# Kernel optimization log

Hardware: AMD Instinct MI355X
Metric: run time of the kernel (lower is better)

Reference implementation:

```python
import jax, jax.numpy as jnp
import numpy as np

B, S, D = 2, 2048, 2560
H, HD = 32, 80           # n_head, head_dim = n_embd // n_head
RD = 32                  # rotary_dim (partial rotary, phi-style)
ROPE_BASE = 10000.0


def _rope_cache(seqlen, rotary_dim):
    # inv_freq = 1 / base^(2i/d); freqs = outer(t, inv_freq)  -> [S, RD//2]
    inv_freq = 1.0 / (ROPE_BASE ** (jnp.arange(0, rotary_dim, 2, dtype=jnp.float32) / rotary_dim))
    t = jnp.arange(seqlen, dtype=jnp.float32)
    freqs = jnp.outer(t, inv_freq)
    return jnp.cos(freqs), jnp.sin(freqs)


def setup_inputs() -> dict:
    key = jax.random.key(0)
    k0, k1, k2, k3, k4 = jax.random.split(key, 5)
    x = jax.random.normal(k0, (B, S, D), dtype=jnp.float32)
    wqkv_w = jax.random.normal(k1, (3 * D, D), dtype=jnp.float32) * 0.02
    wqkv_b = jax.random.normal(k2, (3 * D,), dtype=jnp.float32) * 0.02
    out_w = jax.random.normal(k3, (D, D), dtype=jnp.float32) * 0.02
    out_b = jax.random.normal(k4, (D,), dtype=jnp.float32) * 0.02
    return {"x": x, "wqkv_w": wqkv_w, "wqkv_b": wqkv_b, "out_w": out_w, "out_b": out_b}


def _attention_core(x, wqkv_w, wqkv_b, out_w, out_b):
    b, s, d = x.shape
    qkv = (x @ wqkv_w.T + wqkv_b).reshape(b, s, 3, H, HD)  # [B,S,3,H,HD]

    cos, sin = _rope_cache(s, RD)            # [S, RD//2]
    c = cos[:, None, :]                       # [S,1,RD//2]
    si = sin[:, None, :]

    def rot(t):  # partial NeoX-style rotary on first RD dims; t: [B,S,H,HD]
        t_rot, t_pass = t[..., :RD], t[..., RD:]
        t1, t2 = t_rot[..., : RD // 2], t_rot[..., RD // 2 :]
        return jnp.concatenate([t1 * c - t2 * si, t1 * si + t2 * c, t_pass], axis=-1)

    q = rot(qkv[:, :, 0])                     # [B,S,H,HD]
    k = rot(qkv[:, :, 1])
    v = qkv[:, :, 2]

    # fp32 scores = q @ (k * scale)^T, causal mask filled with -10000.0 (as in source)
    scale = 1.0 / np.sqrt(HD).astype(np.float32)
    scores = jnp.einsum("bqhd,bkhd->bhqk", q, k * scale)  # [B,H,S,S]
    causal_mask = jnp.arange(s)[None, :] > jnp.arange(s)[:, None]  # cols > rows
    scores = jnp.where(causal_mask, jnp.float32(-10000.0), scores)
    attn = jax.nn.softmax(scores, axis=-1)
    ctx = jnp.einsum("bhqk,bkhd->bqhd", attn, v).reshape(b, s, d)
    return ctx @ out_w.T + out_b


def reference(x, wqkv_w, wqkv_b, out_w, out_b):
    return _attention_core(x, wqkv_w, wqkv_b, out_w, out_b)
```

## Files before the change

### kernel.cpp

```cpp
#include <hip/hip_runtime.h>
#include <cstdint>
#include <cstddef>

#define B_  2
#define S_  2048
#define D_  2560
#define H_  32
#define HD_ 80

typedef __attribute__((ext_vector_type(8))) short  short8;
typedef __attribute__((ext_vector_type(4))) float  floatx4;

__device__ __forceinline__ float b2f(unsigned short u) {
  union { unsigned int i; float f; } x; x.i = ((unsigned int)u) << 16; return x.f;
}
__device__ __forceinline__ unsigned short f2bf(float f) {
  union { float f; unsigned int i; } x; x.f = f;
  unsigned int u = x.i;
  return (unsigned short)((u + 0x7fffu + ((u >> 16) & 1u)) >> 16);
}

__global__ void cvt_kernel(const float* __restrict__ in, unsigned short* __restrict__ out, int n4) {
  int i = blockIdx.x * 256 + threadIdx.x;
  if (i >= n4) return;
  const float4 v = ((const float4*)in)[i];
  ushort4 r;
  r.x = f2bf(v.x); r.y = f2bf(v.y); r.z = f2bf(v.z); r.w = f2bf(v.w);
  ((ushort4*)out)[i] = r;
}

#define GLOAD_LDS16(g, l)                                                      \
  __builtin_amdgcn_global_load_lds(                                            \
      (const __attribute__((address_space(1))) void*)(g),                      \
      (__attribute__((address_space(3))) void*)(l), 16, 0, 0)

template <int OUT_BF16>
__global__ __launch_bounds__(256)
void gemm_bt(const unsigned short* __restrict__ A,
             const unsigned short* __restrict__ B,
             const float* __restrict__ bias,
             void* __restrict__ Cv,
             const int M, const int N, const int K) {
  __shared__ unsigned short As[128 * 32];
  __shared__ unsigned short Bs[128 * 32];
  const int tid  = threadIdx.x;
  const int wave = tid >> 6;
  const int lane = tid & 63;
  const int wm   = (wave & 1) << 6;
  const int wn   = (wave >> 1) << 6;
  const int row0 = (int)blockIdx.y << 7;
  const int col0 = (int)blockIdx.x << 7;
  const unsigned short* Ab = A + (size_t)row0 * K;
  const unsigned short* Bb = B + (size_t)col0 * K;
  const int srow = wave * 16 + (lane >> 2);
  const int scol = (lane & 3) << 3;
  const int fr = lane & 15;
  const int fq = (lane >> 4) << 3;
  floatx4 acc[4][4] = {};

  for (int k0 = 0; k0 < K; k0 += 32) {
    __syncthreads();
    GLOAD_LDS16(Ab + (size_t)srow        * K + (k0 + scol), &As[wave * 512]);
    GLOAD_LDS16(Ab + (size_t)(srow + 64) * K + (k0 + scol), &As[2048 + wave * 512]);
    GLOAD_LDS16(Bb + (size_t)srow        * K + (k0 + scol), &Bs[wave * 512]);
    GLOAD_LDS16(Bb + (size_t)(srow + 64) * K + (k0 + scol), &Bs[2048 + wave * 512]);
    __syncthreads();
    short8 aF[4], bF[4];
#pragma unroll
    for (int i = 0; i < 4; i++) aF[i] = *(const short8*)(&As[(wm + i * 16 + fr) * 32 + fq]);
#pragma unroll
    for (int i = 0; i < 4; i++) bF[i] = *(const short8*)(&Bs[(wn + i * 16 + fr) * 32 + fq]);
#pragma unroll
    for (int mi = 0; mi < 4; mi++)
#pragma unroll
      for (int ni = 0; ni < 4; ni++)
        acc[mi][ni] = __builtin_amdgcn_mfma_f32_16x16x32_bf16(aF[mi], bF[ni], acc[mi][ni], 0, 0, 0);
  }

  const int cr = (lane >> 4) << 2;
  const int cn = lane & 15;
  unsigned short* Cb = (unsigned short*)Cv;
  float* Cf = (float*)Cv;
#pragma unroll
  for (int ni = 0; ni < 4; ni++) {
    const int col = col0 + wn + ni * 16 + cn;
    const float bv = bias[col];
#pragma unroll
    for (int mi = 0; mi < 4; mi++) {
      const int rowb = row0 + wm + mi * 16 + cr;
#pragma unroll
      for (int r = 0; r < 4; r++) {
        const float v = acc[mi][ni][r] + bv;
        const size_t idx = (size_t)(rowb + r) * N + col;
        if (OUT_BF16) Cb[idx] = f2bf(v);
        else          Cf[idx] = v;
      }
    }
  }
}

__global__ void rope_kernel(const unsigned short* __restrict__ qkv,
                            unsigned short* __restrict__ Q,
                            unsigned short* __restrict__ K) {
  const int idx = blockIdx.x * 256 + threadIdx.x;
  if (idx >= B_ * S_ * H_) return;
  const int h = idx & (H_ - 1);
  const int s = (idx >> 5) & (S_ - 1);
  const int b = idx >> 16;
  const unsigned short* row = qkv + (size_t)(b * S_ + s) * (3 * D_);
  const size_t obase = ((size_t)(b * H_ + h) * S_ + s) * HD_;

  float cc[16], ssn[16];
#pragma unroll
  for (int i = 0; i < 16; i++) {
    const float ang = (float)s * exp2f((float)i * -0.83048202372184059f);
    ssn[i] = sinf(ang);
    cc[i]  = cosf(ang);
  }
  {
    const float QS = 0.11180339887498949f * 1.4426950408889634f;
    const uint4* src = (const uint4*)(row + h * HD_);
    float f[80], g[80];
#pragma unroll
    for (int i = 0; i < 10; i++) {
      uint4 t = src[i];
      const unsigned short* w = (const unsigned short*)&t;
#pragma unroll
      for (int j = 0; j < 8; j++) f[i * 8 + j] = b2f(w[j]);
    }
#pragma unroll
    for (int i = 0; i < 16; i++) {
      g[i]      = f[i] * cc[i] - f[i + 16] * ssn[i];
      g[i + 16] = f[i] * ssn[i] + f[i + 16] * cc[i];
    }
#pragma unroll
    for (int i = 32; i < 80; i++) g[i] = f[i];
    uint4* dst = (uint4*)(Q + obase);
#pragma unroll
    for (int i = 0; i < 10; i++) {
      uint4 t;
      unsigned short* w = (unsigned short*)&t;
#pragma unroll
      for (int j = 0; j < 8; j++) w[j] = f2bf(g[i * 8 + j] * QS);
      dst[i] = t;
    }
  }
  {
    const uint4* src = (const uint4*)(row + (H_ + h) * HD_);
    float f[32], g[32];
#pragma unroll
    for (int i = 0; i < 4; i++) {
      uint4 t = src[i];
      const unsigned short* w = (const unsigned short*)&t;
#pragma unroll
      for (int j = 0; j < 8; j++) f[i * 8 + j] = b2f(w[j]);
    }
#pragma unroll
    for (int i = 0; i < 16; i++) {
      g[i]      = f[i] * cc[i] - f[i + 16] * ssn[i];
      g[i + 16] = f[i] * ssn[i] + f[i + 16] * cc[i];
    }
    uint4* dst = (uint4*)(K + obase);
#pragma unroll
    for (int i = 0; i < 4; i++) {
      uint4 t;
      unsigned short* w = (unsigned short*)&t;
#pragma unroll
      for (int j = 0; j < 8; j++) w[j] = f2bf(g[i * 8 + j]);
      dst[i] = t;
    }
#pragma unroll
    for (int i = 4; i < 10; i++) dst[i] = src[i];
  }
}

__global__ __launch_bounds__(256)
void vtrans_kernel(const unsigned short* __restrict__ qkv, unsigned short* __restrict__ Vt) {
  __shared__ unsigned short T[64][88];
  const int tid = threadIdx.x;
  const int bh = blockIdx.y;
  const int b = bh >> 5, h = bh & 31;
  const int tile = blockIdx.x;
  const int s0 = tile * 64;
  for (int t = tid; t < 640; t += 256) {
    const int r = t / 10, c = t % 10;
    const size_t src = ((size_t)((b * S_ + s0 + r) * 3) + 2) * D_ + h * HD_ + c * 8;
    *(uint4*)&T[r][c * 8] = *(const uint4*)&qkv[src];
  }
  __syncthreads();
  unsigned short* tb = Vt + ((size_t)bh * 32 + tile) * (80 * 72);
  for (int t = tid; t < 640; t += 256) {
    const int d = t / 8, sc = t % 8;
    uint4 o;
    unsigned short* w = (unsigned short*)&o;
#pragma unroll
    for (int j = 0; j < 8; j++) w[j] = T[sc * 8 + j][d];
    *(uint4*)&tb[d * 72 + sc * 8] = o;
  }
}

__global__ __launch_bounds__(256, 4)
void attn_mfma(const unsigned short* __restrict__ Qg,
               const unsigned short* __restrict__ Kg,
               const unsigned short* __restrict__ Vtg,
               unsigned short* __restrict__ ctx) {
  __shared__ unsigned short Ks[64 * 80];
  __shared__ unsigned short Vs[80 * 72];
  __shared__ unsigned short Ps[4][32 * 72];

  const int tid  = threadIdx.x;
  const int wave = tid >> 6;
  const int lane = tid & 63;
  const int fr   = lane & 15;
  const int fg   = lane >> 4;
  const int bh   = blockIdx.y;
  const int qt   = (int)gridDim.x - 1 - (int)blockIdx.x;
  const int qbase = (qt << 7) + wave * 32;

  const unsigned short* Qrow  = Qg  + (size_t)bh * S_ * HD_;
  const unsigned short* Krow  = Kg  + (size_t)bh * S_ * HD_;
  const unsigned short* Vtile = Vtg + (size_t)bh * 32 * (80 * 72);

  short8 qf[2][3];
  const short8 zfrag = {};
#pragma unroll
  for (int mi = 0; mi < 2; mi++) {
    const unsigned short* qp = Qrow + (size_t)(qbase + mi * 16 + fr) * HD_;
    qf[mi][0] = *(const short8*)&qp[fg * 8];
    qf[mi][1] = *(const short8*)&qp[32 + fg * 8];
    qf[mi][2] = (fg < 2) ? *(const short8*)&qp[64 + fg * 8] : zfrag;
  }

  floatx4 accO[2][5] = {};
  float l_part[2][4] = {};

  const int nch = 2 * qt + 2;
  for (int c = 0; c < nch; c++) {
    const int k0 = c * 64;
    __syncthreads();
    {
      const unsigned short* Kt = Krow + (size_t)k0 * HD_;
      for (int i = wave; i < 10; i += 4)
        GLOAD_LDS16(Kt + i * 512 + lane * 8, &Ks[i * 512]);
    }
    {
      const unsigned short* Vt = Vtile + (size_t)c * (80 * 72);
      for (int i = wave; i < 12; i += 4) {
        const int off = (i < 11) ? i * 512 : 5248;
        GLOAD_LDS16(Vt + off + lane * 8, &Vs[off]);
      }
    }
    __syncthreads();

    floatx4 accS[2][4] = {};
#pragma unroll
    for (int ni = 0; ni < 4; ni++) {
      const unsigned short* kp = &Ks[(ni * 16 + fr) * 80];
      const short8 kf0 = *(const short8*)&kp[fg * 8];
      const short8 kf1 = *(const short8*)&kp[32 + fg * 8];
      const short8 kf2 = *(const short8*)&kp[64 + (fg & 1) * 8];
      accS[0][ni] = __builtin_amdgcn_mfma_f32_16x16x32_bf16(qf[0][0], kf0, accS[0][ni], 0, 0, 0);
      accS[1][ni] = __builtin_amdgcn_mfma_f32_16x16x32_bf16(qf[1][0], kf0, accS[1][ni], 0, 0, 0);
      accS[0][ni] = __builtin_amdgcn_mfma_f32_16x16x32_bf16(qf[0][1], kf1, accS[0][ni], 0, 0, 0);
      accS[1][ni] = __builtin_amdgcn_mfma_f32_16x16x32_bf16(qf[1][1], kf1, accS[1][ni], 0, 0, 0);
      accS[0][ni] = __builtin_amdgcn_mfma_f32_16x16x32_bf16(qf[0][2], kf2, accS[0][ni], 0, 0, 0);
      accS[1][ni] = __builtin_amdgcn_mfma_f32_16x16x32_bf16(qf[1][2], kf2, accS[1][ni], 0, 0, 0);
    }

    if (k0 + 63 > qbase) {
#pragma unroll
      for (int mi = 0; mi < 2; mi++)
#pragma unroll
        for (int ni = 0; ni < 4; ni++)
#pragma unroll
          for (int r = 0; r < 4; r++) {
            const int qg = qbase + mi * 16 + fg * 4 + r;
            const int kg = k0 + ni * 16 + fr;
            if (kg > qg) accS[mi][ni][r] = -1e30f;
          }
    }

#pragma unroll
    for (int mi = 0; mi < 2; mi++)
#pragma unroll
      for (int ni = 0; ni < 4; ni++)
#pragma unroll
        for (int r = 0; r < 4; r++) {
          const float p = __builtin_amdgcn_exp2f(accS[mi][ni][r]);
          l_part[mi][r] += p;
          const int prow = mi * 16 + fg * 4 + r;
          const int pcol = (ni * 16 + fr) ^ (fg << 3);
          Ps[wave][prow * 72 + pcol] = f2bf(p);
        }

#pragma unroll
    for (int kstep = 0; kstep < 2; kstep++) {
      short8 pf[2];
#pragma unroll
      for (int mi = 0; mi < 2; mi++) {
        const int prow = mi * 16 + fr;
        const int pcol = (kstep * 32 + fg * 8) ^ ((fr >> 2) << 3);
        pf[mi] = *(const short8*)&Ps[wave][prow * 72 + pcol];
      }
#pragma unroll
      for (int dt = 0; dt < 5; dt++) {
        const short8 vf = *(const short8*)&Vs[(dt * 16 + fr) * 72 + kstep * 32 + fg * 8];
        accO[0][dt] = __builtin_amdgcn_mfma_f32_16x16x32_bf16(pf[0], vf, accO[0][dt], 0, 0, 0);
        accO[1][dt] = __builtin_amdgcn_mfma_f32_16x16x32_bf16(pf[1], vf, accO[1][dt], 0, 0, 0);
      }
    }
  }

  const int b = bh >> 5, h = bh & 31;
#pragma unroll
  for (int mi = 0; mi < 2; mi++) {
    float inv[4];
#pragma unroll
    for (int r = 0; r < 4; r++) {
      float s = l_part[mi][r];
      s += __shfl_xor(s, 1);
      s += __shfl_xor(s, 2);
      s += __shfl_xor(s, 4);
      s += __shfl_xor(s, 8);
      inv[r] = 1.f / s;
    }
#pragma unroll
    for (int dt = 0; dt < 5; dt++) {
      const int d = dt * 16 + fr;
#pragma unroll
      for (int r = 0; r < 4; r++) {
        const int q = qbase + mi * 16 + fg * 4 + r;
        ctx[(size_t)(b * S_ + q) * D_ + h * HD_ + d] = f2bf(accO[mi][dt][r] * inv[r]);
      }
    }
  }
}

extern "C" void kernel_launch(void* const* d_in, const int* in_sizes, int n_in,
                              void* d_out, int out_size, void* d_ws, size_t ws_size,
                              hipStream_t stream) {
  (void)in_sizes; (void)n_in; (void)out_size; (void)ws_size;
  const float* x      = (const float*)d_in[0];
  const float* wqkv_w = (const float*)d_in[1];
  const float* wqkv_b = (const float*)d_in[2];
  const float* out_w  = (const float*)d_in[3];
  const float* out_b  = (const float*)d_in[4];
  char* ws = (char*)d_ws;

  unsigned short* Xb    = (unsigned short*)(ws + 0);
  unsigned short* Wqkvb = (unsigned short*)(ws + 20971520);
  unsigned short* qkv   = (unsigned short*)(ws + 60293120);
  unsigned short* Qb    = (unsigned short*)(ws + 123207680);
  unsigned short* Kb    = (unsigned short*)(ws + 144179200);
  unsigned short* ctx   = Xb;
  unsigned short* Woutb = Wqkvb;
  unsigned short* Vtile = (unsigned short*)(ws + 34078720);

  cvt_kernel<<<10240, 256, 0, stream>>>(x, Xb, 2621440);
  cvt_kernel<<<19200, 256, 0, stream>>>(wqkv_w, Wqkvb, 4915200);
  gemm_bt<1><<<dim3(60, 32), 256, 0, stream>>>(Xb, Wqkvb, wqkv_b, (void*)qkv, 4096, 7680, 2560);
  rope_kernel<<<512, 256, 0, stream>>>(qkv, Qb, Kb);
  vtrans_kernel<<<dim3(32, 64), 256, 0, stream>>>(qkv, Vtile);
  cvt_kernel<<<6400, 256, 0, stream>>>(out_w, Woutb, 1638400);
  attn_mfma<<<dim3(16, 64), 256, 0, stream>>>(Qb, Kb, Vtile, ctx);
  gemm_bt<0><<<dim3(20, 32), 256, 0, stream>>>(ctx, Woutb, out_b, d_out, 4096, 2560, 2560);
}
```

Baseline: 674.0 us.

## Transpose MFMA operands for vectorized stores, swizzle V tiles, merge conversions

After: 694.2 us. 3.0% more time.

```diff
diff --git a/kernel.cpp b/kernel.cpp
--- a/kernel.cpp
+++ b/kernel.cpp
@@ -20,13 +20,21 @@
   return (unsigned short)((u + 0x7fffu + ((u >> 16) & 1u)) >> 16);
 }
 
-__global__ void cvt_kernel(const float* __restrict__ in, unsigned short* __restrict__ out, int n4) {
-  int i = blockIdx.x * 256 + threadIdx.x;
-  if (i >= n4) return;
-  const float4 v = ((const float4*)in)[i];
+__global__ void cvt3_kernel(const float* __restrict__ s0, unsigned short* __restrict__ d0, int n0,
+                            const float* __restrict__ s1, unsigned short* __restrict__ d1, int n1,
+                            const float* __restrict__ s2, unsigned short* __restrict__ d2, int n2) {
+  int j = blockIdx.x * 256 + threadIdx.x;
+  const float* s; unsigned short* d;
+  if (j < n0) { s = s0; d = d0; }
+  else {
+    j -= n0;
+    if (j < n1) { s = s1; d = d1; }
+    else { j -= n1; if (j >= n2) return; s = s2; d = d2; }
+  }
+  const float4 v = ((const float4*)s)[j];
   ushort4 r;
   r.x = f2bf(v.x); r.y = f2bf(v.y); r.z = f2bf(v.z); r.w = f2bf(v.w);
-  ((ushort4*)out)[i] = r;
+  ((ushort4*)d)[j] = r;
 }
 
 #define GLOAD_LDS16(g, l)                                                      \
@@ -74,26 +82,31 @@
     for (int mi = 0; mi < 4; mi++)
 #pragma unroll
       for (int ni = 0; ni < 4; ni++)
-        acc[mi][ni] = __builtin_amdgcn_mfma_f32_16x16x32_bf16(aF[mi], bF[ni], acc[mi][ni], 0, 0, 0);
-  }
-
-  const int cr = (lane >> 4) << 2;
-  const int cn = lane & 15;
+        acc[mi][ni] = __builtin_amdgcn_mfma_f32_16x16x32_bf16(bF[ni], aF[mi], acc[mi][ni], 0, 0, 0);
+  }
+
+  const int fg = lane >> 4;
   unsigned short* Cb = (unsigned short*)Cv;
   float* Cf = (float*)Cv;
 #pragma unroll
-  for (int ni = 0; ni < 4; ni++) {
-    const int col = col0 + wn + ni * 16 + cn;
-    const float bv = bias[col];
-#pragma unroll
-    for (int mi = 0; mi < 4; mi++) {
-      const int rowb = row0 + wm + mi * 16 + cr;
-#pragma unroll
-      for (int r = 0; r < 4; r++) {
-        const float v = acc[mi][ni][r] + bv;
-        const size_t idx = (size_t)(rowb + r) * N + col;
-        if (OUT_BF16) Cb[idx] = f2bf(v);
-        else          Cf[idx] = v;
+  for (int mi = 0; mi < 4; mi++) {
+    const size_t rowoff = (size_t)(row0 + wm + mi * 16 + fr) * N;
+#pragma unroll
+    for (int ni = 0; ni < 4; ni++) {
+      const int nbase = col0 + wn + ni * 16 + fg * 4;
+      const float4 bv = *(const float4*)&bias[nbase];
+      float v0 = acc[mi][ni][0] + bv.x;
+      float v1 = acc[mi][ni][1] + bv.y;
+      float v2 = acc[mi][ni][2] + bv.z;
+      float v3 = acc[mi][ni][3] + bv.w;
+      if (OUT_BF16) {
+        uint2 w;
+        w.x = (unsigned)f2bf(v0) | ((unsigned)f2bf(v1) << 16);
+        w.y = (unsigned)f2bf(v2) | ((unsigned)f2bf(v3) << 16);
+        *(uint2*)&Cb[rowoff + nbase] = w;
+      } else {
+        float4 w; w.x = v0; w.y = v1; w.z = v2; w.w = v3;
+        *(float4*)&Cf[rowoff + nbase] = w;
       }
     }
   }
@@ -188,14 +201,14 @@
     *(uint4*)&T[r][c * 8] = *(const uint4*)&qkv[src];
   }
   __syncthreads();
-  unsigned short* tb = Vt + ((size_t)bh * 32 + tile) * (80 * 72);
+  unsigned short* tb = Vt + ((size_t)bh * 32 + tile) * 5120;
   for (int t = tid; t < 640; t += 256) {
     const int d = t / 8, sc = t % 8;
     uint4 o;
     unsigned short* w = (unsigned short*)&o;
 #pragma unroll
     for (int j = 0; j < 8; j++) w[j] = T[sc * 8 + j][d];
-    *(uint4*)&tb[d * 72 + sc * 8] = o;
+    *(uint4*)&tb[d * 64 + ((sc * 8) ^ ((d & 7) * 8))] = o;
   }
 }
 
@@ -205,8 +218,8 @@
                const unsigned short* __restrict__ Vtg,
                unsigned short* __restrict__ ctx) {
   __shared__ unsigned short Ks[64 * 80];
-  __shared__ unsigned short Vs[80 * 72];
-  __shared__ unsigned short Ps[4][32 * 72];
+  __shared__ unsigned short Vs[80 * 64];
+  __shared__ unsigned short Ts[4][32 * 40];
 
   const int tid  = threadIdx.x;
   const int wave = tid >> 6;
@@ -219,7 +232,7 @@
 
   const unsigned short* Qrow  = Qg  + (size_t)bh * S_ * HD_;
   const unsigned short* Krow  = Kg  + (size_t)bh * S_ * HD_;
-  const unsigned short* Vtile = Vtg + (size_t)bh * 32 * (80 * 72);
+  const unsigned short* Vtile = Vtg + (size_t)bh * 32 * 5120;
 
   short8 qf[2][3];
   const short8 zfrag = {};
@@ -231,8 +244,8 @@
     qf[mi][2] = (fg < 2) ? *(const short8*)&qp[64 + fg * 8] : zfrag;
   }
 
-  floatx4 accO[2][5] = {};
-  float l_part[2][4] = {};
+  floatx4 accOT[5][2] = {};
+  float l_part[2] = {0.f, 0.f};
 
   const int nch = 2 * qt + 2;
   for (int c = 0; c < nch; c++) {
@@ -244,94 +257,89 @@
         GLOAD_LDS16(Kt + i * 512 + lane * 8, &Ks[i * 512]);
     }
     {
-      const unsigned short* Vt = Vtile + (size_t)c * (80 * 72);
-      for (int i = wave; i < 12; i += 4) {
-        const int off = (i < 11) ? i * 512 : 5248;
-        GLOAD_LDS16(Vt + off + lane * 8, &Vs[off]);
-      }
+      const unsigned short* Vt = Vtile + (size_t)c * 5120;
+      for (int i = wave; i < 10; i += 4)
+        GLOAD_LDS16(Vt + i * 512 + lane * 8, &Vs[i * 512]);
     }
     __syncthreads();
 
-    floatx4 accS[2][4] = {};
+    floatx4 accST[4][2] = {};
 #pragma unroll
     for (int ni = 0; ni < 4; ni++) {
       const unsigned short* kp = &Ks[(ni * 16 + fr) * 80];
       const short8 kf0 = *(const short8*)&kp[fg * 8];
       const short8 kf1 = *(const short8*)&kp[32 + fg * 8];
       const short8 kf2 = *(const short8*)&kp[64 + (fg & 1) * 8];
-      accS[0][ni] = __builtin_amdgcn_mfma_f32_16x16x32_bf16(qf[0][0], kf0, accS[0][ni], 0, 0, 0);
-      accS[1][ni] = __builtin_amdgcn_mfma_f32_16x16x32_bf16(qf[1][0], kf0, accS[1][ni], 0, 0, 0);
-      accS[0][ni] = __builtin_amdgcn_mfma_f32_16x16x32_bf16(qf[0][1], kf1, accS[0][ni], 0, 0, 0);
-      accS[1][ni] = __builtin_amdgcn_mfma_f32_16x16x32_bf16(qf[1][1], kf1, accS[1][ni], 0, 0, 0);
-      accS[0][ni] = __builtin_amdgcn_mfma_f32_16x16x32_bf16(qf[0][2], kf2, accS[0][ni], 0, 0, 0);
-      accS[1][ni] = __builtin_amdgcn_mfma_f32_16x16x32_bf16(qf[1][2], kf2, accS[1][ni], 0, 0, 0);
+      accST[ni][0] = __builtin_amdgcn_mfma_f32_16x16x32_bf16(kf0, qf[0][0], accST[ni][0], 0, 0, 0);
+      accST[ni][1] = __builtin_amdgcn_mfma_f32_16x16x32_bf16(kf0, qf[1][0], accST[ni][1], 0, 0, 0);
+      accST[ni][0] = __builtin_amdgcn_mfma_f32_16x16x32_bf16(kf1, qf[0][1], accST[ni][0], 0, 0, 0);
+      accST[ni][1] = __builtin_amdgcn_mfma_f32_16x16x32_bf16(kf1, qf[1][1], accST[ni][1], 0, 0, 0);
+      accST[ni][0] = __builtin_amdgcn_mfma_f32_16x16x32_bf16(kf2, qf[0][2], accST[ni][0], 0, 0, 0);
+      accST[ni][1] = __builtin_amdgcn_mfma_f32_16x16x32_bf16(kf2, qf[1][2], accST[ni][1], 0, 0, 0);
     }
 
     if (k0 + 63 > qbase) {
 #pragma unroll
-      for (int mi = 0; mi < 2; mi++)
-#pragma unroll
-        for (int ni = 0; ni < 4; ni++)
+      for (int ni = 0; ni < 4; ni++)
+#pragma unroll
+        for (int mi = 0; mi < 2; mi++) {
+          const int qg = qbase + mi * 16 + fr;
 #pragma unroll
           for (int r = 0; r < 4; r++) {
-            const int qg = qbase + mi * 16 + fg * 4 + r;
-            const int kg = k0 + ni * 16 + fr;
-            if (kg > qg) accS[mi][ni][r] = -1e30f;
+            const int kg = k0 + ni * 16 + fg * 4 + r;
+            if (kg > qg) accST[ni][mi][r] = -1e30f;
           }
-    }
-
-#pragma unroll
-    for (int mi = 0; mi < 2; mi++)
-#pragma unroll
-      for (int ni = 0; ni < 4; ni++)
-#pragma unroll
-        for (int r = 0; r < 4; r++) {
-          const float p = __builtin_amdgcn_exp2f(accS[mi][ni][r]);
-          l_part[mi][r] += p;
-          const int prow = mi * 16 + fg * 4 + r;
-          const int pcol = (ni * 16 + fr) ^ (fg << 3);
-          Ps[wave][prow * 72 + pcol] = f2bf(p);
         }
-
-#pragma unroll
-    for (int kstep = 0; kstep < 2; kstep++) {
-      short8 pf[2];
-#pragma unroll
-      for (int mi = 0; mi < 2; mi++) {
-        const int prow = mi * 16 + fr;
-        const int pcol = (kstep * 32 + fg * 8) ^ ((fr >> 2) << 3);
-        pf[mi] = *(const short8*)&Ps[wave][prow * 72 + pcol];
+    }
+
+#pragma unroll
+    for (int hh = 0; hh < 2; hh++) {
+#pragma unroll
+      for (int nh = 0; nh < 2; nh++) {
+        const int ni = hh * 2 + nh;
+#pragma unroll
+        for (int mi = 0; mi < 2; mi++) {
+          const float p0 = __builtin_amdgcn_exp2f(accST[ni][mi][0]);
+          const float p1 = __builtin_amdgcn_exp2f(accST[ni][mi][1]);
+          const float p2 = __builtin_amdgcn_exp2f(accST[ni][mi][2]);
+          const float p3 = __builtin_amdgcn_exp2f(accST[ni][mi][3]);
+          l_part[mi] += (p0 + p1) + (p2 + p3);
+          uint2 w;
+          w.x = (unsigned)f2bf(p0) | ((unsigned)f2bf(p1) << 16);
+          w.y = (unsigned)f2bf(p2) | ((unsigned)f2bf(p3) << 16);
+          *(uint2*)&Ts[wave][(mi * 16 + fr) * 40 + nh * 16 + fg * 4] = w;
+        }
       }
+      const short8 pf0 = *(const short8*)&Ts[wave][fr * 40 + fg * 8];
+      const short8 pf1 = *(const short8*)&Ts[wave][(16 + fr) * 40 + fg * 8];
+      const int vcol = hh * 32 + fg * 8;
 #pragma unroll
       for (int dt = 0; dt < 5; dt++) {
-        const short8 vf = *(const short8*)&Vs[(dt * 16 + fr) * 72 + kstep * 32 + fg * 8];
-        accO[0][dt] = __builtin_amdgcn_mfma_f32_16x16x32_bf16(pf[0], vf, accO[0][dt], 0, 0, 0);
-        accO[1][dt] = __builtin_amdgcn_mfma_f32_16x16x32_bf16(pf[1], vf, accO[1][dt], 0, 0, 0);
+        const short8 vf = *(const short8*)&Vs[(dt * 16 + fr) * 64 + (vcol ^ ((fr & 7) * 8))];
+        accOT[dt][0] = __builtin_amdgcn_mfma_f32_16x16x32_bf16(vf, pf0, accOT[dt][0], 0, 0, 0);
+        accOT[dt][1] = __builtin_amdgcn_mfma_f32_16x16x32_bf16(vf, pf1, accOT[dt][1], 0, 0, 0);
       }
     }
   }
 
-  const int b = bh >> 5, h = bh & 31;
+  const int b = bh >> 5, h2 = bh & 31;
 #pragma unroll
   for (int mi = 0; mi < 2; mi++) {
-    float inv[4];
-#pragma unroll
-    for (int r = 0; r < 4; r++) {
-      float s = l_part[mi][r];
-      s += __shfl_xor(s, 1);
-      s += __shfl_xor(s, 2);
-      s += __shfl_xor(s, 4);
-      s += __shfl_xor(s, 8);
-      inv[r] = 1.f / s;
-    }
+    float s = l_part[mi];
+    s += __shfl_xor(s, 16);
+    s += __shfl_xor(s, 32);
+    const float inv = 1.f / s;
+    const size_t rowoff = (size_t)(b * S_ + qbase + mi * 16 + fr) * D_ + h2 * HD_;
 #pragma unroll
     for (int dt = 0; dt < 5; dt++) {
-      const int d = dt * 16 + fr;
-#pragma unroll
-      for (int r = 0; r < 4; r++) {
-        const int q = qbase + mi * 16 + fg * 4 + r;
-        ctx[(size_t)(b * S_ + q) * D_ + h * HD_ + d] = f2bf(accO[mi][dt][r] * inv[r]);
-      }
+      const float v0 = accOT[dt][mi][0] * inv;
+      const float v1 = accOT[dt][mi][1] * inv;
+      const float v2 = accOT[dt][mi][2] * inv;
+      const float v3 = accOT[dt][mi][3] * inv;
+      uint2 w;
+      w.x = (unsigned)f2bf(v0) | ((unsigned)f2bf(v1) << 16);
+      w.y = (unsigned)f2bf(v2) | ((unsigned)f2bf(v3) << 16);
+      *(uint2*)&ctx[rowoff + dt * 16 + fg * 4] = w;
     }
   }
 }
@@ -352,16 +360,16 @@
   unsigned short* qkv   = (unsigned short*)(ws + 60293120);
   unsigned short* Qb    = (unsigned short*)(ws + 123207680);
   unsigned short* Kb    = (unsigned short*)(ws + 144179200);
+  unsigned short* Woutb = (unsigned short*)(ws + 165150720);
   unsigned short* ctx   = Xb;
-  unsigned short* Woutb = Wqkvb;
   unsigned short* Vtile = (unsigned short*)(ws + 34078720);
 
-  cvt_kernel<<<10240, 256, 0, stream>>>(x, Xb, 2621440);
-  cvt_kernel<<<19200, 256, 0, stream>>>(wqkv_w, Wqkvb, 4915200);
+  cvt3_kernel<<<35840, 256, 0, stream>>>(x, Xb, 2621440,
+                                         wqkv_w, Wqkvb, 4915200,
+                                         out_w, Woutb, 1638400);
   gemm_bt<1><<<dim3(60, 32), 256, 0, stream>>>(Xb, Wqkvb, wqkv_b, (void*)qkv, 4096, 7680, 2560);
   rope_kernel<<<512, 256, 0, stream>>>(qkv, Qb, Kb);
   vtrans_kernel<<<dim3(32, 64), 256, 0, stream>>>(qkv, Vtile);
-  cvt_kernel<<<6400, 256, 0, stream>>>(out_w, Woutb, 1638400);
   attn_mfma<<<dim3(16, 64), 256, 0, stream>>>(Qb, Kb, Vtile, ctx);
   gemm_bt<0><<<dim3(20, 32), 256, 0, stream>>>(ctx, Woutb, out_b, d_out, 4096, 2560, 2560);
 }
```
